# Performance work log

Hardware: AMD Instinct MI355X
Metric: run time of the kernel (lower is better)

The kernel has to match this reference:

```python
import jax, jax.numpy as jnp
import numpy as np

WINDOW_SIZE = 11
CHANNEL = 1
SIGMA = 1.5


def _gaussian_1d(size, sigma):
    coords = jnp.arange(size, dtype=jnp.float32) - size // 2
    g = jnp.exp(-coords ** 2 / (2 * sigma ** 2))
    return g / g.sum()


def _window_3d(size, channel, sigma=SIGMA):
    g = _gaussian_1d(size, sigma)
    w3 = g[:, None, None] * g[None, :, None] * g[None, None, :]  # [K,K,K]
    # OIDHW with groups=channel -> [channel, 1, K, K, K]
    return jnp.broadcast_to(w3[None, None], (channel, 1, size, size, size))


def _conv3d(x, window, channel):
    pad = WINDOW_SIZE // 2
    return jax.lax.conv_general_dilated(
        x, window,
        window_strides=(1, 1, 1),
        padding=[(pad, pad)] * 3,
        dimension_numbers=('NCDHW', 'OIDHW', 'NCDHW'),
        feature_group_count=channel,
    )


def setup_inputs() -> dict:
    key = jax.random.key(0)
    k1, k2 = jax.random.split(key)
    shape = (4, 1, 128, 128, 128)
    img1 = jax.random.uniform(k1, shape, dtype=jnp.float32)
    img2 = jax.random.uniform(k2, shape, dtype=jnp.float32)
    return {"img1": img1, "img2": img2}


def reference(img1, img2):
    channel = img1.shape[1]
    window = _window_3d(WINDOW_SIZE, channel).astype(img1.dtype)

    mu1 = _conv3d(img1, window, channel)
    mu2 = _conv3d(img2, window, channel)
    mu1_sq = mu1 * mu1
    mu2_sq = mu2 * mu2
    mu1_mu2 = mu1 * mu2

    sigma1_sq = _conv3d(img1 * img1, window, channel) - mu1_sq
    sigma2_sq = _conv3d(img2 * img2, window, channel) - mu2_sq
    sigma12 = _conv3d(img1 * img2, window, channel) - mu1_mu2

    C1 = 0.01 ** 2
    C2 = 0.03 ** 2
    ssim_map = ((2 * mu1_mu2 + C1) * (2 * sigma12 + C2)) / (
        (mu1_sq + mu2_sq + C1) * (sigma1_sq + sigma2_sq + C2))
    return ssim_map.mean()
```

## Files before the change

### kernel.cpp

```cpp
#include <hip/hip_runtime.h>
#include <hip/hip_fp16.h>
#include <math.h>

#define NB  4
#define DD  128
#define HH  128
#define WW  128
#define KS  11
#define PAD 5
#define NF  4
#define ZCK 32
#define HCK 32
#define RW  144
#define LOFF 6

using f32x2 = __attribute__((ext_vector_type(2))) float;

struct GW { float g[KS]; };

static __device__ __forceinline__ f32x2 vfma2(f32x2 a, f32x2 b, f32x2 c) {
    return __builtin_elementwise_fma(a, b, c);
}

#define ZSTRIDE (HH * NF * WW)
#define HSTRIDE (NF * WW)

__global__ __launch_bounds__(256)
void k1_wd(const float* __restrict__ img1, const float* __restrict__ img2,
           __half* __restrict__ A, GW gw) {
    __shared__ alignas(16) float srow[2][2][4][RW];
    const int t  = threadIdx.x;
    const int b  = blockIdx.x;
    const int hb = b & 31;
    const int zc = (b >> 5) & 3;
    const int n  = b >> 7;
    const int r  = t >> 6;
    const int q  = t & 63;
    const int w0 = q * 2;
    const int h  = hb * 4 + r;
    const int z0 = zc * ZCK;

    if (t < 192) {
        const int grp = t / 12, s12 = t % 12;
        const int slot = (s12 < 6) ? s12 : (128 + s12);
        srow[grp >> 3][(grp >> 2) & 1][grp & 3][slot] = 0.f;
    }

    const long long inBase  = (long long)n * DD * HH * WW +
                              (long long)h * WW + w0;
    const long long outBase = (long long)n * DD * ZSTRIDE +
                              (long long)h * HSTRIDE + w0;

    f32x2 acc[NF][KS];
    #pragma unroll
    for (int f = 0; f < NF; ++f)
        #pragma unroll
        for (int j = 0; j < KS; ++j) acc[f][j] = (f32x2){0.f, 0.f};

    const int STEPS = ZCK + 2 * PAD;

    float2 rx0 = make_float2(0.f, 0.f), ry0 = rx0, rx1 = rx0, ry1 = rx0;
    {
        const int zi0 = z0 - PAD;
        if (zi0 >= 0) {
            const long long off = inBase + (long long)zi0 * (HH * WW);
            rx0 = *(const float2*)(img1 + off);
            ry0 = *(const float2*)(img2 + off);
        }
        const int zi1 = z0 - PAD + 1;
        if (zi1 >= 0) {
            const long long off = inBase + (long long)zi1 * (HH * WW);
            rx1 = *(const float2*)(img1 + off);
            ry1 = *(const float2*)(img2 + off);
        }
    }
    *(float2*)&srow[0][0][r][LOFF + w0] = rx0;
    *(float2*)&srow[0][1][r][LOFF + w0] = ry0;
    __syncthreads();

    #define ELV(A2, i) ((i) & 1 ? A2[(i) >> 1].y : A2[(i) >> 1].x)

    #define K1_STEP(S, CUR, NXT, RXC, RYC, RXN, RYN, DOST)                     \
    {                                                                          \
        {          \
            const int zi = z0 - PAD + (S) + 2;                                 \
            float2 lx = make_float2(0.f, 0.f), ly = lx;                        \
            if ((S) + 2 < STEPS && zi >= 0 && zi < DD) {                       \
                const long long off = inBase + (long long)zi * (HH * WW);      \
                lx = *(const float2*)(img1 + off);                             \
                ly = *(const float2*)(img2 + off);                             \
            }                                                                  \
            RXC = lx; RYC = ly;                                                \
        }                                                                      \
                  \
        f32x2 xv2[7], yv2[7];                                                  \
        _Pragma("unroll")                                                      \
        for (int i = 0; i < 7; ++i) {                                          \
            const float2 ax = *(const float2*)&srow[CUR][0][r][w0 + 2 * i];    \
            const float2 ay = *(const float2*)&srow[CUR][1][r][w0 + 2 * i];    \
            xv2[i] = (f32x2){ax.x, ax.y};                                      \
            yv2[i] = (f32x2){ay.x, ay.y};                                      \
        }                                                                      \
                                    \
        f32x2 pv2[7], qv2[7];                                                  \
        _Pragma("unroll")                                                      \
        for (int i = 0; i < 7; ++i) {                                          \
            pv2[i] = xv2[i] * yv2[i];                                          \
            qv2[i] = vfma2(yv2[i], yv2[i], xv2[i] * xv2[i]);                   \
        }                                                                      \
                            \
        float a0x = 0.f, a0y = 0.f, a1x = 0.f, a1y = 0.f;                      \
        float a2x = 0.f, a2y = 0.f, a3x = 0.f, a3y = 0.f;                      \
        _Pragma("unroll")                                                      \
        for (int k = 0; k < KS; ++k) {                                         \
            const float g = gw.g[k];                                           \
            a0x = fmaf(g, ELV(xv2, k + 1), a0x);                               \
            a0y = fmaf(g, ELV(xv2, k + 2), a0y);                               \
            a1x = fmaf(g, ELV(yv2, k + 1), a1x);                               \
            a1y = fmaf(g, ELV(yv2, k + 2), a1y);                               \
            a2x = fmaf(g, ELV(pv2, k + 1), a2x);                               \
            a2y = fmaf(g, ELV(pv2, k + 2), a2y);                               \
            a3x = fmaf(g, ELV(qv2, k + 1), a3x);                               \
            a3y = fmaf(g, ELV(qv2, k + 2), a3y);                               \
        }                                                                      \
                                             \
        *(float2*)&srow[NXT][0][r][LOFF + w0] = RXN;                           \
        *(float2*)&srow[NXT][1][r][LOFF + w0] = RYN;                           \
        __syncthreads();                                                       \
                                   \
        f32x2 v[NF];                                                           \
        v[0] = (f32x2){a0x, a0y}; v[1] = (f32x2){a1x, a1y};                    \
        v[2] = (f32x2){a2x, a2y}; v[3] = (f32x2){a3x, a3y};                    \
        _Pragma("unroll")                                                      \
        for (int f = 0; f < NF; ++f) {                                         \
            _Pragma("unroll")                                                  \
            for (int j = KS - 1; j >= 1; --j) {                                \
                const f32x2 gg = {gw.g[j], gw.g[j]};                           \
                acc[f][j] = vfma2(gg, v[f], acc[f][j - 1]);                    \
            }                                                                  \
            const f32x2 g0 = {gw.g[0], gw.g[0]};                               \
            acc[f][0] = g0 * v[f];                                             \
        }                                                                      \
        if (DOST) {                                                            \
            const int zo = z0 + (S) - 2 * PAD;                                 \
            __half* op = A + outBase + (long long)zo * ZSTRIDE;                \
            *(__half2*)(op + 0 * WW) =                                         \
                __float22half2_rn(make_float2(acc[0][KS-1].x, acc[0][KS-1].y));\
            *(__half2*)(op + 1 * WW) =                                         \
                __float22half2_rn(make_float2(acc[1][KS-1].x, acc[1][KS-1].y));\
            *(__half2*)(op + 2 * WW) =                                         \
                __float22half2_rn(make_float2(acc[2][KS-1].x, acc[2][KS-1].y));\
            *(__half2*)(op + 3 * WW) =                                         \
                __float22half2_rn(make_float2(acc[3][KS-1].x, acc[3][KS-1].y));\
        }                                                                      \
    }

    for (int s2 = 0; s2 < 2 * PAD; s2 += 2) {
        K1_STEP(s2,     0, 1, rx0, ry0, rx1, ry1, 0)
        K1_STEP(s2 + 1, 1, 0, rx1, ry1, rx0, ry0, 0)
    }
    for (int s2 = 2 * PAD; s2 < STEPS; s2 += 2) {
        K1_STEP(s2,     0, 1, rx0, ry0, rx1, ry1, 1)
        K1_STEP(s2 + 1, 1, 0, rx1, ry1, rx0, ry0, 1)
    }
    #undef K1_STEP
    #undef ELV
}

__global__ __launch_bounds__(256)
void k2_hssim(const __half* __restrict__ A, double* __restrict__ partials,
              GW gw) {
    const int t  = threadIdx.x;
    const int b  = blockIdx.x;
    const int hc = b & 3;
    const int zp = (b >> 2) & 31;
    const int n  = b >> 7;
    const int zl = t >> 6;
    const int q  = t & 63;
    const int w0 = q * 2;
    const int z  = zp * 4 + zl;
    const int h0 = hc * HCK;

    const long long colBase = ((long long)(n * DD + z)) * ZSTRIDE + w0;

    f32x2 acc[NF][KS];
    #pragma unroll
    for (int f = 0; f < NF; ++f)
        #pragma unroll
        for (int j = 0; j < KS; ++j) acc[f][j] = (f32x2){0.f, 0.f};

    const int STEPS = HCK + 2 * PAD;

    unsigned pfA[NF] = {0u, 0u, 0u, 0u};
    unsigned pfB[NF] = {0u, 0u, 0u, 0u};
    {
        const int hi0 = h0 - PAD;
        if (hi0 >= 0) {
            const __half* p = A + colBase + (long long)hi0 * HSTRIDE;
            #pragma unroll
            for (int f = 0; f < NF; ++f) pfA[f] = *(const unsigned*)(p + f * WW);
        }
        const int hi1 = h0 - PAD + 1;
        if (hi1 >= 0) {
            const __half* p = A + colBase + (long long)hi1 * HSTRIDE;
            #pragma unroll
            for (int f = 0; f < NF; ++f) pfB[f] = *(const unsigned*)(p + f * WW);
        }
    }

    const f32x2 C1v = {1e-4f, 1e-4f}, C2v = {9e-4f, 9e-4f};
    const f32x2 TWO = {2.f, 2.f};
    f32x2 sum = {0.f, 0.f};

    #define K2_STEP(S, PFC, DOSSIM)                                            \
    {                                                                          \
        f32x2 v[NF];                                                           \
        _Pragma("unroll")                                                      \
        for (int f = 0; f < NF; ++f) {                                         \
            const float2 fv = __half22float2(*(const __half2*)&PFC[f]);        \
            v[f] = (f32x2){fv.x, fv.y};                                        \
        }                                                                      \
        {                                                \
            const int hi = h0 - PAD + (S) + 2;                                 \
            _Pragma("unroll")                                                  \
            for (int f = 0; f < NF; ++f) PFC[f] = 0u;                          \
            if ((S) + 2 < STEPS && hi >= 0 && hi < HH) {                       \
                const __half* p = A + colBase + (long long)hi * HSTRIDE;       \
                _Pragma("unroll")                                              \
                for (int f = 0; f < NF; ++f)                                   \
                    PFC[f] = *(const unsigned*)(p + f * WW);                   \
            }                                                                  \
        }                                                                      \
        _Pragma("unroll")                                                      \
        for (int f = 0; f < NF; ++f) {                                         \
            _Pragma("unroll")                                                  \
            for (int j = KS - 1; j >= 1; --j) {                                \
                const f32x2 gg = {gw.g[j], gw.g[j]};                           \
                acc[f][j] = vfma2(gg, v[f], acc[f][j - 1]);                    \
            }                                                                  \
            const f32x2 g0 = {gw.g[0], gw.g[0]};                               \
            acc[f][0] = g0 * v[f];                                             \
        }                                                                      \
        if (DOSSIM) {                                                          \
            const f32x2 mu1 = acc[0][KS - 1], mu2 = acc[1][KS - 1];            \
            const f32x2 mu1s = mu1 * mu1, mu2s = mu2 * mu2, mu12 = mu1 * mu2;  \
            const f32x2 sg12 = acc[2][KS - 1] - mu12;                          \
            const f32x2 sgss = acc[3][KS - 1] - mu1s - mu2s;                   \
            const f32x2 num = vfma2(TWO, mu12, C1v) * vfma2(TWO, sg12, C2v);   \
            const f32x2 den = (mu1s + mu2s + C1v) * (sgss + C2v);              \
            f32x2 rr;                                                          \
            rr.x = __builtin_amdgcn_rcpf(den.x);                               \
            rr.y = __builtin_amdgcn_rcpf(den.y);                               \
            rr = rr * vfma2(-den, rr, TWO);                     \
            sum = vfma2(num, rr, sum);                                         \
        }                                                                      \
    }

    for (int s2 = 0; s2 < 2 * PAD; s2 += 2) {
        K2_STEP(s2,     pfA, 0)
        K2_STEP(s2 + 1, pfB, 0)
    }
    for (int s2 = 2 * PAD; s2 < STEPS; s2 += 2) {
        K2_STEP(s2,     pfA, 1)
        K2_STEP(s2 + 1, pfB, 1)
    }
    #undef K2_STEP

    __shared__ double red[256];
    red[t] = (double)sum.x + (double)sum.y;
    __syncthreads();
    for (int sft = 128; sft > 0; sft >>= 1) {
        if (t < sft) red[t] += red[t + sft];
        __syncthreads();
    }
    if (t == 0) partials[b] = red[0];
}

__global__ __launch_bounds__(256)
void k4_reduce(const double* __restrict__ partials, int nPart,
               float* __restrict__ out) {
    __shared__ double red[256];
    const int t = threadIdx.x;
    double s = 0.0;
    for (int i = t; i < nPart; i += 256) s += partials[i];
    red[t] = s;
    __syncthreads();
    for (int sft = 128; sft > 0; sft >>= 1) {
        if (t < sft) red[t] += red[t + sft];
        __syncthreads();
    }
    if (t == 0) out[0] = (float)(red[0] / (double)((long long)NB * DD * HH * WW));
}

extern "C" void kernel_launch(void* const* d_in, const int* in_sizes, int n_in,
                              void* d_out, int out_size, void* d_ws, size_t ws_size,
                              hipStream_t stream) {
    const float* img1 = (const float*)d_in[0];
    const float* img2 = (const float*)d_in[1];
    float* out = (float*)d_out;

    GW gw;
    {
        double gs[KS], ssum = 0.0;
        for (int i = 0; i < KS; ++i) {
            const double c = (double)(i - KS / 2);
            gs[i] = exp(-c * c / (2.0 * 1.5 * 1.5));
            ssum += gs[i];
        }
        for (int i = 0; i < KS; ++i) gw.g[i] = (float)(gs[i] / ssum);
    }

    __half* A = (__half*)d_ws;
    double* partials =
        (double*)((char*)d_ws + (long long)NB * DD * ZSTRIDE * sizeof(__half));

    const int nBlocksK1 = NB * 32 * (DD / ZCK);
    const int nBlocksK2 = NB * 32 * (HH / HCK);

    k1_wd<<<nBlocksK1, 256, 0, stream>>>(img1, img2, A, gw);
    k2_hssim<<<nBlocksK2, 256, 0, stream>>>(A, partials, gw);
    k4_reduce<<<1, 256, 0, stream>>>(partials, nBlocksK2, out);
}
```

Baseline: 60.65 us.

## Interleave intermediate features for 16-byte accesses and drop block barriers

Reorders the fp16 intermediate buffer so each thread's four feature pairs are contiguous, turning four 4-byte stores and loads into one 16-byte store and load. In the first kernel, each wave now zero-fills and uses only its own shared-memory row, so the block-wide barriers are replaced with a per-wave LDS wait. This is meant to cut memory transaction count and barrier stalls. It relies on wave-synchronous execution for correctness of the shared-row handoff.

New measurement: 58.27 us. 1.04x faster.

```diff
diff --git a/kernel.cpp b/kernel.cpp
--- a/kernel.cpp
+++ b/kernel.cpp
@@ -14,6 +14,10 @@
 #define RW  144
 #define LOFF 6
 
+#define QS      8
+#define HROW    (64 * QS)
+#define ZPLANE  (HH * HROW)
+
 using f32x2 = __attribute__((ext_vector_type(2))) float;
 
 struct GW { float g[KS]; };
@@ -21,9 +25,16 @@
 static __device__ __forceinline__ f32x2 vfma2(f32x2 a, f32x2 b, f32x2 c) {
     return __builtin_elementwise_fma(a, b, c);
 }
-
-#define ZSTRIDE (HH * NF * WW)
-#define HSTRIDE (NF * WW)
+static __device__ __forceinline__ unsigned h2u(__half2 v) {
+    union { __half2 h; unsigned u; } x; x.h = v; return x.u;
+}
+static __device__ __forceinline__ f32x2 u2f2(unsigned u) {
+    union { unsigned u; __half2 h; } x; x.u = u;
+    const float2 f = __half22float2(x.h);
+    return (f32x2){f.x, f.y};
+}
+
+#define WAVE_LDS_FENCE() asm volatile("s_waitcnt lgkmcnt(0)" ::: "memory")
 
 __global__ __launch_bounds__(256)
 void k1_wd(const float* __restrict__ img1, const float* __restrict__ img2,
@@ -40,16 +51,16 @@
     const int h  = hb * 4 + r;
     const int z0 = zc * ZCK;
 
-    if (t < 192) {
-        const int grp = t / 12, s12 = t % 12;
+    if (q < 48) {
+        const int grp = q / 12, s12 = q % 12;
         const int slot = (s12 < 6) ? s12 : (128 + s12);
-        srow[grp >> 3][(grp >> 2) & 1][grp & 3][slot] = 0.f;
+        srow[grp >> 1][grp & 1][r][slot] = 0.f;
     }
 
     const long long inBase  = (long long)n * DD * HH * WW +
                               (long long)h * WW + w0;
-    const long long outBase = (long long)n * DD * ZSTRIDE +
-                              (long long)h * HSTRIDE + w0;
+    const long long outBase = (long long)n * DD * ZPLANE +
+                              (long long)h * HROW + (long long)q * QS;
 
     f32x2 acc[NF][KS];
     #pragma unroll
@@ -76,13 +87,14 @@
     }
     *(float2*)&srow[0][0][r][LOFF + w0] = rx0;
     *(float2*)&srow[0][1][r][LOFF + w0] = ry0;
-    __syncthreads();
 
     #define ELV(A2, i) ((i) & 1 ? A2[(i) >> 1].y : A2[(i) >> 1].x)
 
     #define K1_STEP(S, CUR, NXT, RXC, RYC, RXN, RYN, DOST)                     \
     {                                                                          \
-        {          \
+              \
+        WAVE_LDS_FENCE();                                                      \
+        {           \
             const int zi = z0 - PAD + (S) + 2;                                 \
             float2 lx = make_float2(0.f, 0.f), ly = lx;                        \
             if ((S) + 2 < STEPS && zi >= 0 && zi < DD) {                       \
@@ -92,7 +104,7 @@
             }                                                                  \
             RXC = lx; RYC = ly;                                                \
         }                                                                      \
-                  \
+             \
         f32x2 xv2[7], yv2[7];                                                  \
         _Pragma("unroll")                                                      \
         for (int i = 0; i < 7; ++i) {                                          \
@@ -123,10 +135,9 @@
             a3x = fmaf(g, ELV(qv2, k + 1), a3x);                               \
             a3y = fmaf(g, ELV(qv2, k + 2), a3y);                               \
         }                                                                      \
-                                             \
+              \
         *(float2*)&srow[NXT][0][r][LOFF + w0] = RXN;                           \
         *(float2*)&srow[NXT][1][r][LOFF + w0] = RYN;                           \
-        __syncthreads();                                                       \
                                    \
         f32x2 v[NF];                                                           \
         v[0] = (f32x2){a0x, a0y}; v[1] = (f32x2){a1x, a1y};                    \
@@ -143,15 +154,16 @@
         }                                                                      \
         if (DOST) {                                                            \
             const int zo = z0 + (S) - 2 * PAD;                                 \
-            __half* op = A + outBase + (long long)zo * ZSTRIDE;                \
-            *(__half2*)(op + 0 * WW) =                                         \
-                __float22half2_rn(make_float2(acc[0][KS-1].x, acc[0][KS-1].y));\
-            *(__half2*)(op + 1 * WW) =                                         \
-                __float22half2_rn(make_float2(acc[1][KS-1].x, acc[1][KS-1].y));\
-            *(__half2*)(op + 2 * WW) =                                         \
-                __float22half2_rn(make_float2(acc[2][KS-1].x, acc[2][KS-1].y));\
-            *(__half2*)(op + 3 * WW) =                                         \
-                __float22half2_rn(make_float2(acc[3][KS-1].x, acc[3][KS-1].y));\
+            uint4 pk;                                                          \
+            pk.x = h2u(__float22half2_rn(                                      \
+                       make_float2(acc[0][KS-1].x, acc[0][KS-1].y)));          \
+            pk.y = h2u(__float22half2_rn(                                      \
+                       make_float2(acc[1][KS-1].x, acc[1][KS-1].y)));          \
+            pk.z = h2u(__float22half2_rn(                                      \
+                       make_float2(acc[2][KS-1].x, acc[2][KS-1].y)));          \
+            pk.w = h2u(__float22half2_rn(                                      \
+                       make_float2(acc[3][KS-1].x, acc[3][KS-1].y)));          \
+            *(uint4*)(A + outBase + (long long)zo * ZPLANE) = pk;              \
         }                                                                      \
     }
 
@@ -177,11 +189,11 @@
     const int n  = b >> 7;
     const int zl = t >> 6;
     const int q  = t & 63;
-    const int w0 = q * 2;
     const int z  = zp * 4 + zl;
     const int h0 = hc * HCK;
 
-    const long long colBase = ((long long)(n * DD + z)) * ZSTRIDE + w0;
+    const long long colBase =
+        ((long long)(n * DD + z)) * ZPLANE + (long long)q * QS;
 
     f32x2 acc[NF][KS];
     #pragma unroll
@@ -191,21 +203,14 @@
 
     const int STEPS = HCK + 2 * PAD;
 
-    unsigned pfA[NF] = {0u, 0u, 0u, 0u};
-    unsigned pfB[NF] = {0u, 0u, 0u, 0u};
+    uint4 pfA = make_uint4(0u, 0u, 0u, 0u), pfB = pfA;
     {
         const int hi0 = h0 - PAD;
-        if (hi0 >= 0) {
-            const __half* p = A + colBase + (long long)hi0 * HSTRIDE;
-            #pragma unroll
-            for (int f = 0; f < NF; ++f) pfA[f] = *(const unsigned*)(p + f * WW);
-        }
+        if (hi0 >= 0)
+            pfA = *(const uint4*)(A + colBase + (long long)hi0 * HROW);
         const int hi1 = h0 - PAD + 1;
-        if (hi1 >= 0) {
-            const __half* p = A + colBase + (long long)hi1 * HSTRIDE;
-            #pragma unroll
-            for (int f = 0; f < NF; ++f) pfB[f] = *(const unsigned*)(p + f * WW);
-        }
+        if (hi1 >= 0)
+            pfB = *(const uint4*)(A + colBase + (long long)hi1 * HROW);
     }
 
     const f32x2 C1v = {1e-4f, 1e-4f}, C2v = {9e-4f, 9e-4f};
@@ -215,21 +220,14 @@
     #define K2_STEP(S, PFC, DOSSIM)                                            \
     {                                                                          \
         f32x2 v[NF];                                                           \
-        _Pragma("unroll")                                                      \
-        for (int f = 0; f < NF; ++f) {                                         \
-            const float2 fv = __half22float2(*(const __half2*)&PFC[f]);        \
-            v[f] = (f32x2){fv.x, fv.y};                                        \
-        }                                                                      \
+        v[0] = u2f2(PFC.x); v[1] = u2f2(PFC.y);                                \
+        v[2] = u2f2(PFC.z); v[3] = u2f2(PFC.w);                                \
         {                                                \
             const int hi = h0 - PAD + (S) + 2;                                 \
-            _Pragma("unroll")                                                  \
-            for (int f = 0; f < NF; ++f) PFC[f] = 0u;                          \
-            if ((S) + 2 < STEPS && hi >= 0 && hi < HH) {                       \
-                const __half* p = A + colBase + (long long)hi * HSTRIDE;       \
-                _Pragma("unroll")                                              \
-                for (int f = 0; f < NF; ++f)                                   \
-                    PFC[f] = *(const unsigned*)(p + f * WW);                   \
-            }                                                                  \
+            uint4 nv = make_uint4(0u, 0u, 0u, 0u);                             \
+            if ((S) + 2 < STEPS && hi >= 0 && hi < HH)                         \
+                nv = *(const uint4*)(A + colBase + (long long)hi * HROW);      \
+            PFC = nv;                                                          \
         }                                                                      \
         _Pragma("unroll")                                                      \
         for (int f = 0; f < NF; ++f) {                                         \
@@ -312,7 +310,7 @@
 
     __half* A = (__half*)d_ws;
     double* partials =
-        (double*)((char*)d_ws + (long long)NB * DD * ZSTRIDE * sizeof(__half));
+        (double*)((char*)d_ws + (long long)NB * DD * ZPLANE * sizeof(__half));
 
     const int nBlocksK1 = NB * 32 * (DD / ZCK);
     const int nBlocksK2 = NB * 32 * (HH / HCK);
```
